# Kernel tuning notes

Measured on AMD Instinct MI355X. Metric: run time of the kernel, lower is better.

The kernel has to match this reference:

```python
import jax, jax.numpy as jnp
import numpy as np

EPS = 1e-5

def _ln(x):
    # LayerNorm over last dim, no affine (elementwise_affine=False), biased variance
    mu = jnp.mean(x, axis=-1, keepdims=True)
    var = jnp.mean(jnp.square(x - mu), axis=-1, keepdims=True)
    return (x - mu) / jnp.sqrt(var + EPS)

def setup_inputs() -> dict:
    key = jax.random.key(0)
    B, I, H = 32768, 512, 512
    ks = jax.random.split(key, 12)
    std = 1.0 / np.sqrt(H)
    u = lambda k, shape: jax.random.uniform(k, shape, jnp.float32, -std, std)
    return {
        "x": jax.random.normal(ks[0], (B, I), jnp.float32),
        "h": jax.random.normal(ks[1], (B, H), jnp.float32),
        "W_i2h": u(ks[2], (I, 2 * H)),
        "b_i2h": u(ks[3], (2 * H,)),
        "W_h2h": u(ks[4], (H, 2 * H)),
        "b_h2h": u(ks[5], (2 * H,)),
        "W_hatW": u(ks[6], (I, H)),
        "b_hatW": u(ks[7], (H,)),
        "W_hatU": u(ks[8], (H, H)),
        "b_hatU": u(ks[9], (H,)),
    }

def reference(x, h, W_i2h, b_i2h, W_h2h, b_h2h, W_hatW, b_hatW, W_hatU, b_hatU):
    H = W_hatU.shape[0]
    i2h = _ln(x @ W_i2h + b_i2h)          # [B, 2H]
    h2h = _ln(h @ W_h2h + b_h2h)          # [B, 2H]
    gates = jax.nn.sigmoid(i2h + h2h)
    z_t = gates[:, :H]
    r_t = gates[:, -H:]
    h_hat_first = _ln(x @ W_hatW + b_hatW)  # [B, H]
    h_hat_last = _ln(h @ W_hatU + b_hatU)   # [B, H]
    h_hat = jnp.tanh(h_hat_first + r_t * h_hat_last)
    h_t = (1.0 - z_t) * h + z_t * h_hat
    return h_t
```

## Files before the change

### kernel.cpp

```cpp
#include <hip/hip_runtime.h>
#include <stdint.h>

typedef unsigned short u16;
typedef __attribute__((ext_vector_type(8))) short short8;
typedef __attribute__((ext_vector_type(4))) short short4v;
typedef __attribute__((ext_vector_type(4))) float f4;
typedef __attribute__((ext_vector_type(4))) float f32x4;

static __device__ __forceinline__ u16 f2b(float f) {
  union { float f; uint32_t u; } c; c.f = f;
  return (u16)((c.u + 0x7FFFu + ((c.u >> 16) & 1u)) >> 16);
}
static __device__ __forceinline__ float b2f(u16 s) {
  union { uint32_t u; float f; } c; c.u = ((uint32_t)s) << 16; return c.f;
}

__global__ __launch_bounds__(256) void cvt_kernel(const float* __restrict__ x,
                                                  const float* __restrict__ h,
                                                  u16* __restrict__ Ab) {
  const size_t NT = (size_t)4096 * 256;
  bool isH = blockIdx.x >= 4096;
  const float* src = isH ? h : x;
  u16* dst = Ab + (isH ? ((size_t)32768 * 512) : 0);
  size_t t0 = (size_t)(blockIdx.x & 4095) * 256 + threadIdx.x;

  f4 v0 = *(const f4*)(src + ((t0 + 0 * NT) << 2));
  f4 v1 = *(const f4*)(src + ((t0 + 1 * NT) << 2));
  f4 v2 = *(const f4*)(src + ((t0 + 2 * NT) << 2));
  f4 v3 = *(const f4*)(src + ((t0 + 3 * NT) << 2));
  asm volatile("" ::: "memory");

#define CVTST(v, j) do { \
    short4v o; \
    o[0] = (short)f2b((v)[0]); o[1] = (short)f2b((v)[1]); \
    o[2] = (short)f2b((v)[2]); o[3] = (short)f2b((v)[3]); \
    *(short4v*)(dst + ((t0 + (j) * NT) << 2)) = o; \
  } while (0)
  CVTST(v0, 0); CVTST(v1, 1); CVTST(v2, 2); CVTST(v3, 3);
#undef CVTST
}

__global__ __launch_bounds__(256) void transpose_cat(const float* __restrict__ WA0,
                                                     const float* __restrict__ WB0,
                                                     const float* __restrict__ WA1,
                                                     const float* __restrict__ WB1,
                                                     u16* __restrict__ dst0,
                                                     u16* __restrict__ dst1) {
  __shared__ float t[32][33];
  int n0 = blockIdx.x * 32, k0 = blockIdx.y * 32;
  int tx = threadIdx.x, ty = threadIdx.y;
  const float* srcA = blockIdx.z ? WA1 : WA0;
  const float* srcB = blockIdx.z ? WB1 : WB0;
  u16* dst = blockIdx.z ? dst1 : dst0;
  const float* src; int strideN, nb;
  if (n0 < 1024) { src = srcA; strideN = 1024; nb = n0; }
  else           { src = srcB; strideN = 512;  nb = n0 - 1024; }
#pragma unroll
  for (int i = 0; i < 4; ++i) {
    int k = k0 + ty + i * 8;
    t[tx][ty + i * 8] = src[(size_t)k * strideN + nb + tx];
  }
  __syncthreads();
#pragma unroll
  for (int i = 0; i < 4; ++i) {
    int n = ty + i * 8;
    dst[(size_t)(n0 + n) * 512 + k0 + tx] = f2b(t[n][tx]);
  }
}

__global__ __launch_bounds__(256, 2) void gemm_kernel(
    const u16* __restrict__ Ab, const u16* __restrict__ WxT,
    const u16* __restrict__ WhT, u16* __restrict__ Cb,
    int rowStartX, int rowStartH, int tilesPerHalf) {
  __shared__ u16 As[128 * 64];
  __shared__ u16 Bs[128 * 64];

  int nwg = gridDim.x;
  int bid = blockIdx.x;
  int swz = (bid & 7) * (nwg >> 3) + (bid >> 3);
  int mb = swz / 12, nb = swz - mb * 12;
  size_t m0;
  const u16* Wt;
  if (mb < tilesPerHalf) { m0 = (size_t)rowStartX + (size_t)mb * 128; Wt = WxT; }
  else { m0 = (size_t)rowStartH + (size_t)(mb - tilesPerHalf) * 128; Wt = WhT; }
  int crow0 = mb * 128;
  int n0 = nb * 128;

  int tid = threadIdx.x, lane = tid & 63, wv = tid >> 6;
  int wm = wv >> 1, wn = wv & 1;
  int l15 = lane & 15, l4 = lane >> 4, l7 = lane & 7;

  f32x4 acc[4][4] = {};

  int sRow = lane >> 3;
  int g = (lane & 7) ^ sRow;

  for (int kt = 0; kt < 8; ++kt) {
    int k0 = kt << 6;
#pragma unroll
    for (int i = 0; i < 4; ++i) {
      int chunk = wv * 4 + i;
      int rowg = chunk * 8 + sRow;
      const u16* srcA = Ab + (m0 + rowg) * 512 + (k0 + g * 8);
      const u16* srcB = Wt + (size_t)(n0 + rowg) * 512 + (k0 + g * 8);
      __builtin_amdgcn_global_load_lds(
          (const __attribute__((address_space(1))) void*)srcA,
          (__attribute__((address_space(3))) void*)(As + chunk * 512), 16, 0, 0);
      __builtin_amdgcn_global_load_lds(
          (const __attribute__((address_space(1))) void*)srcB,
          (__attribute__((address_space(3))) void*)(Bs + chunk * 512), 16, 0, 0);
    }
    __syncthreads();
#pragma unroll
    for (int ks = 0; ks < 2; ++ks) {
      short8 af[4], bf[4];
#pragma unroll
      for (int mr = 0; mr < 4; ++mr) {
        int r = wm * 64 + mr * 16 + l15;
        int slot = (ks * 4 + l4) ^ l7;
        af[mr] = *(const short8*)(As + r * 64 + slot * 8);
      }
#pragma unroll
      for (int nr = 0; nr < 4; ++nr) {
        int r = wn * 64 + nr * 16 + l15;
        int slot = (ks * 4 + l4) ^ l7;
        bf[nr] = *(const short8*)(Bs + r * 64 + slot * 8);
      }
#pragma unroll
      for (int mr = 0; mr < 4; ++mr)
#pragma unroll
        for (int nr = 0; nr < 4; ++nr)
          acc[mr][nr] = __builtin_amdgcn_mfma_f32_16x16x32_bf16(
              bf[nr], af[mr], acc[mr][nr], 0, 0, 0);
    }
    __syncthreads();
  }

#pragma unroll
  for (int mr = 0; mr < 4; ++mr) {
    int m = crow0 + wm * 64 + mr * 16 + l15;
#pragma unroll
    for (int nr = 0; nr < 4; ++nr) {
      int n = n0 + wn * 64 + nr * 16 + l4 * 4;
      short4v o;
      o[0] = (short)f2b(acc[mr][nr][0]);
      o[1] = (short)f2b(acc[mr][nr][1]);
      o[2] = (short)f2b(acc[mr][nr][2]);
      o[3] = (short)f2b(acc[mr][nr][3]);
      *(short4v*)(Cb + (size_t)m * 1536 + n) = o;
    }
  }
}

__global__ __launch_bounds__(256) void epi_kernel(
    const u16* __restrict__ Cb, const float* __restrict__ h,
    const float* __restrict__ b_i2h, const float* __restrict__ b_h2h,
    const float* __restrict__ b_hatW, const float* __restrict__ b_hatU,
    float* __restrict__ out, int mBase, int BC) {
  int wv = threadIdx.x >> 6;
  int lane = threadIdx.x & 63;
  int mLocal = blockIdx.x * 4 + wv;
  size_t mGlob = (size_t)mBase + mLocal;
  const u16* Ar = Cb + (size_t)mLocal * 1536;
  const u16* Br = Cb + ((size_t)BC + mLocal) * 1536;
  int j0 = lane * 8;

  float a[3][8], b[3][8];
#pragma unroll
  for (int c = 0; c < 3; ++c) {
    short8 va = *(const short8*)(Ar + c * 512 + j0);
    short8 vb = *(const short8*)(Br + c * 512 + j0);
    const float* biasA = (c == 0) ? (b_i2h + j0) : (c == 1) ? (b_i2h + 512 + j0) : (b_hatW + j0);
    const float* biasB = (c == 0) ? (b_h2h + j0) : (c == 1) ? (b_h2h + 512 + j0) : (b_hatU + j0);
    f4 ba0 = *(const f4*)biasA, ba1 = *(const f4*)(biasA + 4);
    f4 bb0 = *(const f4*)biasB, bb1 = *(const f4*)(biasB + 4);
#pragma unroll
    for (int j = 0; j < 4; ++j) {
      a[c][j]     = b2f((u16)va[j])     + ba0[j];
      a[c][j + 4] = b2f((u16)va[j + 4]) + ba1[j];
      b[c][j]     = b2f((u16)vb[j])     + bb0[j];
      b[c][j + 4] = b2f((u16)vb[j + 4]) + bb1[j];
    }
  }

  float s1a = 0, q1a = 0, s2a = 0, q2a = 0, s1b = 0, q1b = 0, s2b = 0, q2b = 0;
#pragma unroll
  for (int j = 0; j < 8; ++j) {
    s1a += a[0][j] + a[1][j]; q1a += a[0][j] * a[0][j] + a[1][j] * a[1][j];
    s2a += a[2][j];           q2a += a[2][j] * a[2][j];
    s1b += b[0][j] + b[1][j]; q1b += b[0][j] * b[0][j] + b[1][j] * b[1][j];
    s2b += b[2][j];           q2b += b[2][j] * b[2][j];
  }
#pragma unroll
  for (int off = 32; off > 0; off >>= 1) {
    s1a += __shfl_xor(s1a, off); q1a += __shfl_xor(q1a, off);
    s2a += __shfl_xor(s2a, off); q2a += __shfl_xor(q2a, off);
    s1b += __shfl_xor(s1b, off); q1b += __shfl_xor(q1b, off);
    s2b += __shfl_xor(s2b, off); q2b += __shfl_xor(q2b, off);
  }
  const float inv1 = 1.0f / 1024.0f, inv2 = 1.0f / 512.0f, eps = 1e-5f;
  float mu1a = s1a * inv1, mu2a = s2a * inv2, mu1b = s1b * inv1, mu2b = s2b * inv2;
  float rs1a = rsqrtf(q1a * inv1 - mu1a * mu1a + eps);
  float rs2a = rsqrtf(q2a * inv2 - mu2a * mu2a + eps);
  float rs1b = rsqrtf(q1b * inv1 - mu1b * mu1b + eps);
  float rs2b = rsqrtf(q2b * inv2 - mu2b * mu2b + eps);

  const float* hrow = h + mGlob * 512 + j0;
  f4 h0 = *(const f4*)hrow, h1 = *(const f4*)(hrow + 4);
  f4 o0, o1;
#pragma unroll
  for (int j = 0; j < 8; ++j) {
    float zs  = (a[0][j] - mu1a) * rs1a + (b[0][j] - mu1b) * rs1b;
    float rsg = (a[1][j] - mu1a) * rs1a + (b[1][j] - mu1b) * rs1b;
    float z = 1.0f / (1.0f + __expf(-zs));
    float r = 1.0f / (1.0f + __expf(-rsg));
    float hh = tanhf((a[2][j] - mu2a) * rs2a + r * ((b[2][j] - mu2b) * rs2b));
    float hv = (j < 4) ? h0[j] : h1[j - 4];
    float o = hv + z * (hh - hv);
    if (j < 4) o0[j] = o; else o1[j - 4] = o;
  }
  *(f4*)(out + mGlob * 512 + j0) = o0;
  *(f4*)(out + mGlob * 512 + j0 + 4) = o1;
}

extern "C" void kernel_launch(void* const* d_in, const int* in_sizes, int n_in,
                              void* d_out, int out_size, void* d_ws, size_t ws_size,
                              hipStream_t stream) {
  const float* x      = (const float*)d_in[0];
  const float* h      = (const float*)d_in[1];
  const float* W_i2h  = (const float*)d_in[2];
  const float* b_i2h  = (const float*)d_in[3];
  const float* W_h2h  = (const float*)d_in[4];
  const float* b_h2h  = (const float*)d_in[5];
  const float* W_hatW = (const float*)d_in[6];
  const float* b_hatW = (const float*)d_in[7];
  const float* W_hatU = (const float*)d_in[8];
  const float* b_hatU = (const float*)d_in[9];
  float* out = (float*)d_out;

  u16* WxT = (u16*)d_ws;
  u16* WhT = WxT + (size_t)1536 * 512;
  u16* Ab  = WhT + (size_t)1536 * 512;
  u16* Cb  = Ab + (size_t)65536 * 512;

  size_t fixedElems = (size_t)2 * 1536 * 512 + (size_t)65536 * 512;
  int chunks = 4;
  for (;;) {
    size_t need = (fixedElems + (size_t)2 * (32768 / chunks) * 1536) * sizeof(u16);
    if (need <= ws_size || chunks >= 128) break;
    chunks <<= 1;
  }
  int BC = 32768 / chunks;
  int tph = BC / 128;
  int nwg = 2 * tph * 12;

  cvt_kernel<<<8192, 256, 0, stream>>>(x, h, Ab);
  transpose_cat<<<dim3(48, 16, 2), dim3(32, 8), 0, stream>>>(
      W_i2h, W_hatW, W_h2h, W_hatU, WxT, WhT);
  for (int cc = 0; cc < chunks; ++cc) {
    gemm_kernel<<<nwg, 256, 0, stream>>>(Ab, WxT, WhT, Cb,
                                         cc * BC, 32768 + cc * BC, tph);
    epi_kernel<<<BC / 4, 256, 0, stream>>>(Cb, h, b_i2h, b_h2h, b_hatW, b_hatU,
                                           out, cc * BC, BC);
  }
}
```

Before: 249.1 us.

## Rewrite GEMM as 256x256 tile, 8-wave double-buffered pipelined kernel

The bf16 GEMM moves from 128x128 tiles with 4 waves and a single LDS buffer to 256x256 tiles with 8 waves. It uses a 128 KB double-buffered LDS ring, loading the next K-slice via global_load_lds while MFMAs run, with explicit vmcnt waits, sched barriers and setprio. Host chunking drops from 4 to 2 chunks so each launch covers more rows. The aim is to hide global-load latency and raise data reuse per tile, at the cost of heavy LDS use, which limits occupancy, and fragile hand scheduling.

```diff
diff --git a/kernel.cpp b/kernel.cpp
--- a/kernel.cpp
+++ b/kernel.cpp
@@ -23,13 +23,11 @@
   const float* src = isH ? h : x;
   u16* dst = Ab + (isH ? ((size_t)32768 * 512) : 0);
   size_t t0 = (size_t)(blockIdx.x & 4095) * 256 + threadIdx.x;
-
   f4 v0 = *(const f4*)(src + ((t0 + 0 * NT) << 2));
   f4 v1 = *(const f4*)(src + ((t0 + 1 * NT) << 2));
   f4 v2 = *(const f4*)(src + ((t0 + 2 * NT) << 2));
   f4 v3 = *(const f4*)(src + ((t0 + 3 * NT) << 2));
   asm volatile("" ::: "memory");
-
 #define CVTST(v, j) do { \
     short4v o; \
     o[0] = (short)f2b((v)[0]); o[1] = (short)f2b((v)[1]); \
@@ -68,77 +66,142 @@
   }
 }
 
-__global__ __launch_bounds__(256, 2) void gemm_kernel(
+#define AS1 __attribute__((address_space(1)))
+#define AS3 __attribute__((address_space(3)))
+#define SBAR0 __builtin_amdgcn_sched_barrier(0)
+#define MF __builtin_amdgcn_mfma_f32_16x16x32_bf16
+
+__global__ __launch_bounds__(512, 2) void gemm_kernel(
     const u16* __restrict__ Ab, const u16* __restrict__ WxT,
     const u16* __restrict__ WhT, u16* __restrict__ Cb,
     int rowStartX, int rowStartH, int tilesPerHalf) {
-  __shared__ u16 As[128 * 64];
-  __shared__ u16 Bs[128 * 64];
-
-  int nwg = gridDim.x;
-  int bid = blockIdx.x;
-  int swz = (bid & 7) * (nwg >> 3) + (bid >> 3);
-  int mb = swz / 12, nb = swz - mb * 12;
-  size_t m0;
-  const u16* Wt;
-  if (mb < tilesPerHalf) { m0 = (size_t)rowStartX + (size_t)mb * 128; Wt = WxT; }
-  else { m0 = (size_t)rowStartH + (size_t)(mb - tilesPerHalf) * 128; Wt = WhT; }
-  int crow0 = mb * 128;
-  int n0 = nb * 128;
+  __shared__ u16 lds[65536];
 
   int tid = threadIdx.x, lane = tid & 63, wv = tid >> 6;
-  int wm = wv >> 1, wn = wv & 1;
+  int wm = wv >> 2, wn = wv & 3;
   int l15 = lane & 15, l4 = lane >> 4, l7 = lane & 7;
 
-  f32x4 acc[4][4] = {};
-
-  int sRow = lane >> 3;
-  int g = (lane & 7) ^ sRow;
-
-  for (int kt = 0; kt < 8; ++kt) {
-    int k0 = kt << 6;
-#pragma unroll
-    for (int i = 0; i < 4; ++i) {
-      int chunk = wv * 4 + i;
-      int rowg = chunk * 8 + sRow;
-      const u16* srcA = Ab + (m0 + rowg) * 512 + (k0 + g * 8);
-      const u16* srcB = Wt + (size_t)(n0 + rowg) * 512 + (k0 + g * 8);
-      __builtin_amdgcn_global_load_lds(
-          (const __attribute__((address_space(1))) void*)srcA,
-          (__attribute__((address_space(3))) void*)(As + chunk * 512), 16, 0, 0);
-      __builtin_amdgcn_global_load_lds(
-          (const __attribute__((address_space(1))) void*)srcB,
-          (__attribute__((address_space(3))) void*)(Bs + chunk * 512), 16, 0, 0);
-    }
-    __syncthreads();
-#pragma unroll
-    for (int ks = 0; ks < 2; ++ks) {
-      short8 af[4], bf[4];
-#pragma unroll
-      for (int mr = 0; mr < 4; ++mr) {
-        int r = wm * 64 + mr * 16 + l15;
-        int slot = (ks * 4 + l4) ^ l7;
-        af[mr] = *(const short8*)(As + r * 64 + slot * 8);
-      }
-#pragma unroll
-      for (int nr = 0; nr < 4; ++nr) {
-        int r = wn * 64 + nr * 16 + l15;
-        int slot = (ks * 4 + l4) ^ l7;
-        bf[nr] = *(const short8*)(Bs + r * 64 + slot * 8);
-      }
-#pragma unroll
-      for (int mr = 0; mr < 4; ++mr)
-#pragma unroll
-        for (int nr = 0; nr < 4; ++nr)
-          acc[mr][nr] = __builtin_amdgcn_mfma_f32_16x16x32_bf16(
-              bf[nr], af[mr], acc[mr][nr], 0, 0, 0);
-    }
-    __syncthreads();
-  }
-
-#pragma unroll
-  for (int mr = 0; mr < 4; ++mr) {
-    int m = crow0 + wm * 64 + mr * 16 + l15;
+  int nwg = gridDim.x, bid = blockIdx.x;
+  int swz = (nwg & 7) ? bid : ((bid & 7) * (nwg >> 3) + (bid >> 3));
+  int mb = swz / 6, nb = swz - mb * 6;
+  size_t m0; const u16* Wt;
+  if (mb < tilesPerHalf) { m0 = (size_t)rowStartX + (size_t)mb * 256; Wt = WxT; }
+  else { m0 = (size_t)rowStartH + (size_t)(mb - tilesPerHalf) * 256; Wt = WhT; }
+  int crow0 = mb * 256, n0 = nb * 256;
+  const u16* At = Ab + m0 * 512;
+  const u16* Bt = Wt + (size_t)n0 * 512;
+
+#define UNIT(tbase, row0, kt, dstoff) do { \
+    _Pragma("unroll") \
+    for (int i_ = 0; i_ < 2; ++i_) { \
+      int si_ = i_ * 512 + tid; \
+      int r_ = si_ >> 3, s_ = si_ & 7; \
+      int g_ = s_ ^ (r_ & 7); \
+      __builtin_amdgcn_global_load_lds( \
+          (const AS1 void*)((tbase) + (size_t)((row0) + r_) * 512 + (kt) * 64 + g_ * 8), \
+          (AS3 void*)(lds + (dstoff) + si_ * 8), 16, 0, 0); \
+    } \
+  } while (0)
+
+#define LDA(bufo, q, mr, ks) \
+  (*(const short8*)(lds + (bufo) + (wm * 128 + (q) * 32 + (mr) * 16 + l15) * 64 + \
+                    ((((ks) * 4 + l4) ^ l7) << 3)))
+#define LDB(bufo, f, ks) \
+  (*(const short8*)(lds + (bufo) + 16384 + (wn * 64 + (f) * 16 + l15) * 64 + \
+                    ((((ks) * 4 + l4) ^ l7) << 3)))
+
+#define BARSEQ do { SBAR0; __builtin_amdgcn_s_barrier(); \
+    asm volatile("s_waitcnt lgkmcnt(0)" ::: "memory"); SBAR0; } while (0)
+
+#define MFMAQ(q, A00, A10, A01, A11) do { \
+    __builtin_amdgcn_s_setprio(1); \
+    _Pragma("unroll") for (int f_ = 0; f_ < 4; ++f_) \
+      acc[(q)*2][f_]   = MF(br[f_][0], A00, acc[(q)*2][f_], 0, 0, 0); \
+    _Pragma("unroll") for (int f_ = 0; f_ < 4; ++f_) \
+      acc[(q)*2+1][f_] = MF(br[f_][0], A10, acc[(q)*2+1][f_], 0, 0, 0); \
+    _Pragma("unroll") for (int f_ = 0; f_ < 4; ++f_) \
+      acc[(q)*2][f_]   = MF(br[f_][1], A01, acc[(q)*2][f_], 0, 0, 0); \
+    _Pragma("unroll") for (int f_ = 0; f_ < 4; ++f_) \
+      acc[(q)*2+1][f_] = MF(br[f_][1], A11, acc[(q)*2+1][f_], 0, 0, 0); \
+    __builtin_amdgcn_s_setprio(0); \
+  } while (0)
+
+#define PH(bufo, q) \
+    short8 a00 = LDA(bufo, q, 0, 0), a10 = LDA(bufo, q, 1, 0), \
+           a01 = LDA(bufo, q, 0, 1), a11 = LDA(bufo, q, 1, 1)
+
+  f32x4 acc[8][4] = {};
+
+  UNIT(At, 0,   0, 0);     UNIT(At, 128, 0, 8192);
+  UNIT(Bt, 0,   0, 16384); UNIT(Bt, 128, 0, 24576);
+  UNIT(Bt, 0,   1, 32768 + 16384); UNIT(Bt, 128, 1, 32768 + 24576);
+  asm volatile("s_waitcnt vmcnt(4)" ::: "memory");
+  SBAR0; __builtin_amdgcn_s_barrier(); SBAR0;
+
+#pragma unroll
+  for (int t = 0; t < 4; ++t) {
+    const int b0 = 0, b1 = 32768;
+    const int k1 = 2 * t + 1;
+    const bool st = (t < 3);
+    short8 br[4][2];
+    {
+#pragma unroll
+      for (int f_ = 0; f_ < 4; ++f_) { br[f_][0] = LDB(b0, f_, 0); br[f_][1] = LDB(b0, f_, 1); }
+      PH(b0, 0);
+      UNIT(At, 0, k1, b1 + 0);
+      BARSEQ; MFMAQ(0, a00, a10, a01, a11);
+    }
+    {
+      PH(b0, 1);
+      UNIT(At, 128, k1, b1 + 8192);
+      BARSEQ; MFMAQ(1, a00, a10, a01, a11);
+    }
+    {
+      PH(b0, 2);
+      if (st) UNIT(Bt, 0, k1 + 1, b0 + 16384);
+      BARSEQ; MFMAQ(2, a00, a10, a01, a11);
+    }
+    {
+      PH(b0, 3);
+      if (st) { UNIT(Bt, 128, k1 + 1, b0 + 24576);
+                asm volatile("s_waitcnt vmcnt(4)" ::: "memory"); }
+      else    { asm volatile("s_waitcnt vmcnt(0)" ::: "memory"); }
+      BARSEQ; MFMAQ(3, a00, a10, a01, a11);
+    }
+    {
+#pragma unroll
+      for (int f_ = 0; f_ < 4; ++f_) { br[f_][0] = LDB(b1, f_, 0); br[f_][1] = LDB(b1, f_, 1); }
+      PH(b1, 0);
+      if (st) UNIT(At, 0, k1 + 1, b0 + 0);
+      BARSEQ; MFMAQ(0, a00, a10, a01, a11);
+    }
+    {
+      PH(b1, 1);
+      if (st) UNIT(At, 128, k1 + 1, b0 + 8192);
+      BARSEQ; MFMAQ(1, a00, a10, a01, a11);
+    }
+    {
+      PH(b1, 2);
+      if (st) UNIT(Bt, 0, k1 + 2, b1 + 16384);
+      BARSEQ; MFMAQ(2, a00, a10, a01, a11);
+    }
+    {
+      PH(b1, 3);
+      if (st) { UNIT(Bt, 128, k1 + 2, b1 + 24576);
+                asm volatile("s_waitcnt vmcnt(4)" ::: "memory"); }
+      BARSEQ; MFMAQ(3, a00, a10, a01, a11);
+    }
+  }
+#undef UNIT
+#undef LDA
+#undef LDB
+#undef BARSEQ
+#undef MFMAQ
+#undef PH
+
+#pragma unroll
+  for (int mr = 0; mr < 8; ++mr) {
+    int m = crow0 + wm * 128 + mr * 16 + l15;
 #pragma unroll
     for (int nr = 0; nr < 4; ++nr) {
       int n = n0 + wn * 64 + nr * 16 + l4 * 4;
@@ -244,21 +307,21 @@
   u16* Cb  = Ab + (size_t)65536 * 512;
 
   size_t fixedElems = (size_t)2 * 1536 * 512 + (size_t)65536 * 512;
-  int chunks = 4;
+  int chunks = 2;
   for (;;) {
     size_t need = (fixedElems + (size_t)2 * (32768 / chunks) * 1536) * sizeof(u16);
     if (need <= ws_size || chunks >= 128) break;
     chunks <<= 1;
   }
   int BC = 32768 / chunks;
-  int tph = BC / 128;
-  int nwg = 2 * tph * 12;
+  int tph = BC / 256;
+  int nwg = 2 * tph * 6;
 
   cvt_kernel<<<8192, 256, 0, stream>>>(x, h, Ab);
   transpose_cat<<<dim3(48, 16, 2), dim3(32, 8), 0, stream>>>(
       W_i2h, W_hatW, W_h2h, W_hatU, WxT, WhT);
   for (int cc = 0; cc < chunks; ++cc) {
-    gemm_kernel<<<nwg, 256, 0, stream>>>(Ab, WxT, WhT, Cb,
+    gemm_kernel<<<nwg, 512, 0, stream>>>(Ab, WxT, WhT, Cb,
                                          cc * BC, 32768 + cc * BC, tph);
     epi_kernel<<<BC / 4, 256, 0, stream>>>(Cb, h, b_i2h, b_h2h, b_hatW, b_hatU,
                                            out, cc * BC, BC);
```

Result: faster. 236.9 us (-4.9%).
